# Kernel optimization log

Measured on AMD Instinct MI355X. Metric: run time of the kernel, lower is better.

Reference implementation:

```python
import jax, jax.numpy as jnp
import numpy as np

BATCH, SEQ = 2, 2048
HID = 2048          # hidden_size
INTER = 4096        # intermediate_size
STATE = 16          # ssm_state_size
RANK = 128          # time_step_rank
K = 4               # conv_kernel


def setup_inputs() -> dict:
    key = jax.random.key(0)
    ks = jax.random.split(key, 8)
    s = 0.02
    return {
        "hidden_states": jax.random.normal(ks[0], (BATCH, SEQ, HID), jnp.float32),
        "in_proj_w": jax.random.normal(ks[1], (2 * INTER, HID), jnp.float32) * s,
        "conv_w": jax.random.normal(ks[2], (INTER, 1, K), jnp.float32) * s,   # depthwise (O, I/g=1, K)
        "conv_b": jnp.zeros((INTER,), jnp.float32),
        "x_proj_w": jax.random.normal(ks[3], (RANK + 2 * STATE, INTER), jnp.float32) * s,
        "dt_proj_w": jax.random.normal(ks[4], (INTER, RANK), jnp.float32) * s,
        "dt_proj_b": jax.random.normal(ks[5], (INTER,), jnp.float32) * s,
        "A_log": jnp.log(jnp.broadcast_to(jnp.arange(1, STATE + 1, dtype=jnp.float32), (INTER, STATE))),
        "D": jnp.ones((INTER,), jnp.float32),
        "out_proj_w": jax.random.normal(ks[6], (HID, INTER), jnp.float32) * s,
    }


def reference(hidden_states, in_proj_w, conv_w, conv_b, x_proj_w,
              dt_proj_w, dt_proj_b, A_log, D, out_proj_w):
    B, L, _ = hidden_states.shape
    # in_proj -> (B, L, 2*INTER), split into u (SSM input) and gate
    proj = jnp.einsum('blh,ph->blp', hidden_states, in_proj_w)
    u, gate = jnp.split(proj, 2, axis=-1)                       # (B, L, INTER) each
    # depthwise causal conv1d on channel-major layout (B, INTER, L)
    uc = jnp.swapaxes(u, 1, 2)
    conv = jax.lax.conv_general_dilated(
        uc, conv_w, window_strides=(1,), padding=[(K - 1, 0)],
        dimension_numbers=('NCH', 'OIH', 'NCH'), feature_group_count=INTER)
    u = jax.nn.silu(conv + conv_b[None, :, None])               # (B, INTER, L)
    # x_proj: dt-rank + B + C, computed in fp32 like the original
    ssm_p = jnp.einsum('bdl,pd->blp', u, x_proj_w).astype(jnp.float32)
    dt_r, Bm, Cm = jnp.split(ssm_p, [RANK, RANK + STATE], axis=-1)  # (B,L,RANK),(B,L,N),(B,L,N)
    dt = jax.nn.softplus(jnp.einsum('blr,dr->bld', dt_r, dt_proj_w) + dt_proj_b)  # (B, L, INTER)
    A = -jnp.exp(A_log)                                         # (INTER, STATE)

    def step(state, xs):
        dt_t, B_t, C_t, u_t = xs                                # (B,D),(B,N),(B,N),(B,D)
        dA = jnp.exp(dt_t[:, :, None] * A[None])                # (B, D, N)
        state = dA * state + (dt_t * u_t)[:, :, None] * B_t[:, None, :]
        y = jnp.einsum('bdn,bn->bd', state, C_t)
        return state, y

    xs = (jnp.swapaxes(dt, 0, 1),        # (L, B, D)
          jnp.swapaxes(Bm, 0, 1),        # (L, B, N)
          jnp.swapaxes(Cm, 0, 1),        # (L, B, N)
          jnp.moveaxis(u, 2, 0))         # (L, B, D)
    init = jnp.zeros((B, INTER, STATE), jnp.float32)
    _, ys = jax.lax.scan(step, init, xs)                        # (L, B, D)

    y = jnp.moveaxis(ys, 0, 1) + jnp.swapaxes(u, 1, 2) * D[None, None, :]  # skip connection
    y = y * jax.nn.silu(gate)
    return jnp.einsum('bld,hd->blh', y, out_proj_w)             # (B, L, HID)
```

## Files before the change

### kernel.cpp

```cpp
#include <hip/hip_runtime.h>

typedef unsigned int u32;
typedef unsigned short u16;
typedef float f32x4 __attribute__((ext_vector_type(4)));
typedef float f32x16 __attribute__((ext_vector_type(16)));
typedef u16 us4 __attribute__((ext_vector_type(4)));
typedef u16 us8 __attribute__((ext_vector_type(8)));
typedef __bf16 bf16x8 __attribute__((ext_vector_type(8)));

__device__ __forceinline__ u16 f2bf(float f) {
  u32 u = __builtin_bit_cast(u32, f);
  u += 0x7fffu + ((u >> 16) & 1u);
  return (u16)(u >> 16);
}
__device__ __forceinline__ float bf2f(u16 h) {
  u32 u = ((u32)h) << 16;
  return __builtin_bit_cast(float, u);
}
__device__ __forceinline__ void async16(const void* g, void* l) {
  __builtin_amdgcn_global_load_lds((const __attribute__((address_space(1))) void*)g,
                                   (__attribute__((address_space(3))) void*)l, 16, 0, 0);
}

#define STG(GP, LP, OFF, KOFF)                              \
  {                                                         \
    async16((GP) + (KOFF), (LP) + (OFF));                   \
    async16((GP) + 128L * K + (KOFF), (LP) + (OFF) + 4096); \
  }

#define PHASE(SET, KS, MH, STAGE_STMT, TAIL_STMT)                               \
  {                                                                             \
    const u16* Ap_ = As + (SET) * 16384 + (KS) * 8192;                          \
    const u16* Bp_ = Bs + (SET) * 16384 + (KS) * 8192;                          \
    us8 af0 = *(const us8*)(Ap_ + ra[(MH) * 4 + 0]);                            \
    us8 af1 = *(const us8*)(Ap_ + ra[(MH) * 4 + 1]);                            \
    us8 af2 = *(const us8*)(Ap_ + ra[(MH) * 4 + 2]);                            \
    us8 af3 = *(const us8*)(Ap_ + ra[(MH) * 4 + 3]);                            \
    if ((MH) == 0) {                                                            \
      _Pragma("unroll") for (int nf = 0; nf < 4; ++nf)                          \
          bfr[nf] = *(const us8*)(Bp_ + rb[nf]);                                \
    }                                                                           \
    STAGE_STMT;                                                                 \
    __builtin_amdgcn_s_barrier();                                               \
    asm volatile("s_waitcnt lgkmcnt(0)" ::: "memory");                          \
    __builtin_amdgcn_sched_barrier(0);                                          \
    __builtin_amdgcn_s_setprio(1);                                              \
    _Pragma("unroll") for (int nf = 0; nf < 4; ++nf) {                          \
      acc[(MH) * 4 + 0][nf] = __builtin_amdgcn_mfma_f32_16x16x32_bf16(          \
          __builtin_bit_cast(bf16x8, af0), __builtin_bit_cast(bf16x8, bfr[nf]), \
          acc[(MH) * 4 + 0][nf], 0, 0, 0);                                      \
      acc[(MH) * 4 + 1][nf] = __builtin_amdgcn_mfma_f32_16x16x32_bf16(          \
          __builtin_bit_cast(bf16x8, af1), __builtin_bit_cast(bf16x8, bfr[nf]), \
          acc[(MH) * 4 + 1][nf], 0, 0, 0);                                      \
      acc[(MH) * 4 + 2][nf] = __builtin_amdgcn_mfma_f32_16x16x32_bf16(          \
          __builtin_bit_cast(bf16x8, af2), __builtin_bit_cast(bf16x8, bfr[nf]), \
          acc[(MH) * 4 + 2][nf], 0, 0, 0);                                      \
      acc[(MH) * 4 + 3][nf] = __builtin_amdgcn_mfma_f32_16x16x32_bf16(          \
          __builtin_bit_cast(bf16x8, af3), __builtin_bit_cast(bf16x8, bfr[nf]), \
          acc[(MH) * 4 + 3][nf], 0, 0, 0);                                      \
    }                                                                           \
    __builtin_amdgcn_s_setprio(0);                                              \
    TAIL_STMT;                                                                  \
    __builtin_amdgcn_s_barrier();                                               \
  }

__global__ __launch_bounds__(512, 2) void gemm256(const u16* __restrict__ A,
                                                  const u16* __restrict__ B,
                                                  u16* __restrict__ U,
                                                  u16* __restrict__ G, int K) {
  __shared__ __align__(16) u16 As[32768];
  __shared__ __align__(16) u16 Bs[32768];
  const int tid = threadIdx.x;
  const int lane = tid & 63;
  const int wave = tid >> 6;
  const int wm = wave >> 2;
  const int wn = wave & 3;
  const int l15 = lane & 15;
  const int kc2 = lane >> 4;
  const int pc2s = kc2 ^ ((l15 >> 1) & 3);

  const int nbx = (int)gridDim.x;
  const int d = (int)blockIdx.y * nbx + (int)blockIdx.x;
  const int cpn = nbx >> 3;
  const int xcd = d & 7;
  const int s = d >> 3;
  const long colBase = (long)(xcd * cpn + (s % cpn)) << 8;
  const long rowBase = (long)(s / cpn) << 8;

  const int c0 = ((tid & 3) ^ ((tid >> 3) & 3)) << 3;
  const u16* Ag = A + (rowBase + (tid >> 2)) * (long)K + c0;
  const u16* Bg = B + (colBase + (tid >> 2)) * (long)K + c0;
  u16* Alds = As + tid * 8;
  u16* Blds = Bs + tid * 8;

  int ra[8], rb[4];
#pragma unroll
  for (int mf = 0; mf < 8; ++mf)
    ra[mf] = (wm * 128 + mf * 16 + l15) * 32 + pc2s * 8;
#pragma unroll
  for (int nf = 0; nf < 4; ++nf)
    rb[nf] = (wn * 64 + nf * 16 + l15) * 32 + pc2s * 8;

  f32x4 acc[8][4] = {};
  us8 bfr[4];

  STG(Ag, Alds, 0, 0);
  STG(Bg, Blds, 0, 0);
  STG(Ag, Alds, 8192, 32);
  STG(Bg, Blds, 8192, 32);
  STG(Ag, Alds, 16384, 64);
  STG(Bg, Blds, 16384, 64);
  asm volatile("s_waitcnt vmcnt(4)" ::: "memory");
  __builtin_amdgcn_s_barrier();

  const int nIter = K >> 7;
  for (int t = 0; t < nIter; ++t) {
    const int k1 = (2 * t + 1) * 64;
    const int k2 = (2 * t + 2) * 64;
    const int k3 = (2 * t + 3) * 64;
    const bool full = (t < nIter - 1);
    PHASE(0, 0, 0, { STG(Ag, Alds, 24576, k1 + 32); }, {});
    PHASE(0, 0, 1, { STG(Bg, Blds, 24576, k1 + 32); },
          { asm volatile("s_waitcnt vmcnt(8)" ::: "memory"); });
    PHASE(0, 1, 0, { if (full) STG(Ag, Alds, 0, k2); }, {});
    PHASE(0, 1, 1, { if (full) STG(Bg, Blds, 0, k2); },
          {
            if (full) asm volatile("s_waitcnt vmcnt(8)" ::: "memory");
            else asm volatile("s_waitcnt vmcnt(4)" ::: "memory");
          });
    PHASE(1, 0, 0, { if (full) STG(Ag, Alds, 8192, k2 + 32); }, {});
    PHASE(1, 0, 1, { if (full) STG(Bg, Blds, 8192, k2 + 32); },
          {
            if (full) asm volatile("s_waitcnt vmcnt(8)" ::: "memory");
            else asm volatile("s_waitcnt vmcnt(0)" ::: "memory");
          });
    PHASE(1, 1, 0, { if (full) STG(Ag, Alds, 16384, k3); }, {});
    PHASE(1, 1, 1, { if (full) STG(Bg, Blds, 16384, k3); },
          { if (full) asm volatile("s_waitcnt vmcnt(8)" ::: "memory"); });
  }

  const int gate = (colBase >= 4096);
  u16* Out = gate ? G : U;
  const long cb = gate ? (colBase - 4096) : colBase;
#pragma unroll
  for (int mf = 0; mf < 8; ++mf) {
    long row0 = rowBase + wm * 128 + mf * 16 + (lane >> 4) * 4;
#pragma unroll
    for (int nf = 0; nf < 4; ++nf) {
      long col = cb + wn * 64 + nf * 16 + l15;
#pragma unroll
      for (int r = 0; r < 4; ++r) {
        float v = acc[mf][nf][r];
        if (gate) v = v / (1.f + __expf(-v));
        Out[(row0 + r) * 4096 + col] = f2bf(v);
      }
    }
  }
}

template <int ACT, bool SPLITK = false>
__global__ __launch_bounds__(256) void gemm_bt(const u16* __restrict__ A,
                                               const u16* __restrict__ B,
                                               void* __restrict__ Cv,
                                               const float* __restrict__ bias,
                                               int K, int ldc) {
  __shared__ __align__(16) u16 As[128 * 64];
  __shared__ __align__(16) u16 Bs[128 * 64];
  const int tid = threadIdx.x;
  const int lane = tid & 63;
  const int wave = tid >> 6;
  const int ln = lane & 31;
  const int hw = lane >> 5;
  const int wm = (wave >> 1) << 6;
  const int wn = (wave & 1) << 6;
  const long rowBase = (long)blockIdx.y << 7;
  const long colBase = (long)blockIdx.x << 7;

  int kStart = 0, kEnd = K;
  if constexpr (SPLITK) {
    int kn = K / gridDim.z;
    kStart = blockIdx.z * kn;
    kEnd = kStart + kn;
  }

  const int rr = tid >> 3;
  const int qg = (tid & 7) ^ (rr & 7);
  const u16* Ag = A + (rowBase + rr) * (long)K + qg * 8;
  const u16* Bg = B + (colBase + rr) * (long)K + qg * 8;
  u16* Al = As + tid * 8;
  u16* Bl = Bs + tid * 8;

  f32x16 acc[2][2] = {};
  const int l7 = ln & 7;

  for (int k0 = kStart; k0 < kEnd; k0 += 64) {
#pragma unroll
    for (int c = 0; c < 4; ++c) {
      async16(Ag + 32L * c * K + k0, Al + 2048 * c);
      async16(Bg + 32L * c * K + k0, Bl + 2048 * c);
    }
    __syncthreads();
#pragma unroll
    for (int s = 0; s < 4; ++s) {
      const int xa = ((s * 2 + hw) ^ l7) * 8;
      us8 af[2], bfr[2];
#pragma unroll
      for (int i = 0; i < 2; ++i)
        af[i] = *(const us8*)(As + (wm + i * 32 + ln) * 64 + xa);
#pragma unroll
      for (int i = 0; i < 2; ++i)
        bfr[i] = *(const us8*)(Bs + (wn + i * 32 + ln) * 64 + xa);
#pragma unroll
      for (int i = 0; i < 2; ++i)
#pragma unroll
        for (int j = 0; j < 2; ++j)
          acc[i][j] = __builtin_amdgcn_mfma_f32_32x32x16_bf16(
              __builtin_bit_cast(bf16x8, af[i]), __builtin_bit_cast(bf16x8, bfr[j]),
              acc[i][j], 0, 0, 0);
    }
    __syncthreads();
  }

  float* Cf = (float*)Cv;
  if constexpr (SPLITK)
    Cf += (size_t)blockIdx.z * ((size_t)gridDim.y * 128 * ldc);

#pragma unroll
  for (int i = 0; i < 2; ++i)
#pragma unroll
    for (int j = 0; j < 2; ++j)
#pragma unroll
      for (int r = 0; r < 16; ++r) {
        long row = rowBase + wm + i * 32 + (r & 3) + 8 * (r >> 2) + 4 * hw;
        long col = colBase + wn + j * 32 + ln;
        float v = acc[i][j][r];
        if constexpr (ACT == 0) {
          Cf[row * ldc + col] = v;
        } else if constexpr (ACT == 3) {
          v += bias[col];
          float sp = (v > 20.f) ? v : log1pf(__expf(v));
          Cf[row * ldc + col] = sp;
        } else if constexpr (ACT == 4) {
          v += bias[col];
          float sp = (v > 20.f) ? v : log1pf(__expf(v));
          ((u16*)Cv)[row * ldc + col] = f2bf(sp);
        }
      }
}

__device__ __forceinline__ void cvt4(const float* __restrict__ in,
                                     u16* __restrict__ out, int i) {
  f32x4 v = ((const f32x4*)in)[i];
  us4 o;
  o[0] = f2bf(v[0]); o[1] = f2bf(v[1]); o[2] = f2bf(v[2]); o[3] = f2bf(v[3]);
  ((us4*)out)[i] = o;
}
__global__ __launch_bounds__(256) void cvt_all(
    const float* __restrict__ hs, const float* __restrict__ wIn,
    const float* __restrict__ wOut, const float* __restrict__ wDt,
    const float* __restrict__ wX, u16* __restrict__ Xb, u16* __restrict__ Winb,
    u16* __restrict__ Wob, u16* __restrict__ Wdtb, u16* __restrict__ Wxb) {
  int i = blockIdx.x * 256 + threadIdx.x;
  if (i < 2097152) { cvt4(hs, Xb, i); return; }
  i -= 2097152;
  if (i < 4194304) { cvt4(wIn, Winb, i); return; }
  i -= 4194304;
  if (i < 2097152) { cvt4(wOut, Wob, i); return; }
  i -= 2097152;
  if (i < 131072) { cvt4(wDt, Wdtb, i); return; }
  i -= 131072;
  if (i >= 262144) return;
  int row = (i << 2) >> 12;
  us4 o;
  if (row < 160) {
    f32x4 v = ((const f32x4*)wX)[i];
    o[0] = f2bf(v[0]); o[1] = f2bf(v[1]); o[2] = f2bf(v[2]); o[3] = f2bf(v[3]);
  } else {
    o[0] = 0; o[1] = 0; o[2] = 0; o[3] = 0;
  }
  ((us4*)Wxb)[i] = o;
}

__global__ __launch_bounds__(256) void xp_reduce(const float* __restrict__ part,
                                                 float* __restrict__ smp,
                                                 u16* __restrict__ dtrb) {
  int i = blockIdx.x * 256 + threadIdx.x;
  const f32x4* p = (const f32x4*)part;
  f32x4 v = p[i];
  v += p[i + 262144];
  v += p[i + 524288];
  v += p[i + 786432];
  ((f32x4*)smp)[i] = v;
  int e = i << 2;
  int c = e & 255;
  if (c < 128) {
    int t = e >> 8;
    us4 o;
    o[0] = f2bf(v[0]); o[1] = f2bf(v[1]); o[2] = f2bf(v[2]); o[3] = f2bf(v[3]);
    *(us4*)(dtrb + t * 128 + c) = o;
  }
}

__global__ __launch_bounds__(256) void conv_silu(const u16* __restrict__ U,
                                                 const float* __restrict__ cw,
                                                 const float* __restrict__ cb,
                                                 u16* __restrict__ out) {
  int i = blockIdx.x * 256 + threadIdx.x;
  int t = i >> 10;
  int d4 = (i & 1023) << 2;
  int l = t & 2047;
  float w[4][4];
#pragma unroll
  for (int j = 0; j < 4; ++j) {
    f32x4 wv = *(const f32x4*)(cw + (d4 + j) * 4);
    w[j][0] = wv[0]; w[j][1] = wv[1]; w[j][2] = wv[2]; w[j][3] = wv[3];
  }
  float r[4] = {cb[d4], cb[d4 + 1], cb[d4 + 2], cb[d4 + 3]};
#pragma unroll
  for (int k = 0; k < 4; ++k) {
    int ll = l - 3 + k;
    if (ll >= 0) {
      us4 xv = *(const us4*)(U + (size_t)(t - 3 + k) * 4096 + d4);
      r[0] += w[0][k] * bf2f(xv[0]);
      r[1] += w[1][k] * bf2f(xv[1]);
      r[2] += w[2][k] * bf2f(xv[2]);
      r[3] += w[3][k] * bf2f(xv[3]);
    }
  }
  us4 o;
#pragma unroll
  for (int j = 0; j < 4; ++j) {
    float v = r[j];
    float s = v / (1.f + __expf(-v));
    o[j] = f2bf(s);
  }
  *(us4*)(out + (size_t)t * 4096 + d4) = o;
}

__global__ __launch_bounds__(256) void scan_part(
    const u16* __restrict__ dt, const u16* __restrict__ ub,
    const float* __restrict__ ssmp, const float* __restrict__ Alog,
    float* __restrict__ Sout, float* __restrict__ dtsumo) {
  const int tid = threadIdx.x;
  const int chunk = blockIdx.x, dgrp = blockIdx.y, b = blockIdx.z;
  const int d = (dgrp << 8) + tid;
  float A[16];
#pragma unroll
  for (int q = 0; q < 4; ++q) {
    f32x4 v = *(const f32x4*)(Alog + d * 16 + q * 4);
    A[q * 4 + 0] = -__expf(v[0]);
    A[q * 4 + 1] = -__expf(v[1]);
    A[q * 4 + 2] = -__expf(v[2]);
    A[q * 4 + 3] = -__expf(v[3]);
  }
  bool fastl = true;
#pragma unroll
  for (int n = 1; n < 16; ++n)
    fastl = fastl && (fabsf(A[n] - (n + 1) * A[0]) <= 1e-4f * (float)(n + 1));
  const bool fast = (__ballot(fastl) == ~0ull);

  const int base = b * 2048 + chunk * 64;
  const u16* dtp = dt + (size_t)base * 4096 + d;
  const u16* up = ub + (size_t)base * 4096 + d;
  const float* Bp = ssmp + (size_t)base * 256 + 128;

  float s[16] = {};
  float dtsum = 0.f;
  float cdt[8], cu[8], ndt[8] = {}, nu[8] = {};
#pragma unroll
  for (int j = 0; j < 8; ++j) {
    cdt[j] = bf2f(dtp[j * 4096]);
    cu[j] = bf2f(up[j * 4096]);
  }
  for (int l0 = 0; l0 < 64; l0 += 8) {
    if (l0 + 8 < 64) {
      int o = (l0 + 8) * 4096;
#pragma unroll
      for (int j = 0; j < 8; ++j) {
        ndt[j] = bf2f(dtp[o + j * 4096]);
        nu[j] = bf2f(up[o + j * 4096]);
      }
    }
    if (fast) {
#pragma unroll
      for (int j = 0; j < 8; ++j) {
        float e1 = __expf(cdt[j] * A[0]);
        float x = cdt[j] * cu[j];
        const float* Bl = Bp + (l0 + j) * 256;
        f32x4 B0 = *(const f32x4*)(Bl);
        f32x4 B1 = *(const f32x4*)(Bl + 4);
        f32x4 B2 = *(const f32x4*)(Bl + 8);
        f32x4 B3 = *(const f32x4*)(Bl + 12);
        float p = 1.f;
#pragma unroll
        for (int n = 0; n < 16; ++n) {
          p *= e1;
          float Bn = (n < 4) ? B0[n & 3] : (n < 8) ? B1[n & 3] : (n < 12) ? B2[n & 3] : B3[n & 3];
          s[n] = fmaf(p, s[n], x * Bn);
        }
        dtsum += cdt[j];
      }
    } else {
#pragma unroll
      for (int j = 0; j < 8; ++j) {
        float x = cdt[j] * cu[j];
        const float* Bl = Bp + (l0 + j) * 256;
        f32x4 B0 = *(const f32x4*)(Bl);
        f32x4 B1 = *(const f32x4*)(Bl + 4);
        f32x4 B2 = *(const f32x4*)(Bl + 8);
        f32x4 B3 = *(const f32x4*)(Bl + 12);
#pragma unroll
        for (int n = 0; n < 16; ++n) {
          float e = __expf(cdt[j] * A[n]);
          float Bn = (n < 4) ? B0[n & 3] : (n < 8) ? B1[n & 3] : (n < 12) ? B2[n & 3] : B3[n & 3];
          s[n] = fmaf(e, s[n], x * Bn);
        }
        dtsum += cdt[j];
      }
    }
#pragma unroll
    for (int j = 0; j < 8; ++j) { cdt[j] = ndt[j]; cu[j] = nu[j]; }
  }
  size_t o = ((size_t)(b * 32 + chunk) * 16) * 4096 + d;
#pragma unroll
  for (int n = 0; n < 16; ++n) Sout[o + (size_t)n * 4096] = s[n];
  dtsumo[(size_t)(b * 32 + chunk) * 4096 + d] = dtsum;
}

__global__ __launch_bounds__(256) void scan_fold(
    const float* __restrict__ Sin, const float* __restrict__ dtsum,
    const float* __restrict__ Alog, float* __restrict__ Sinit) {
  const int tid = threadIdx.x;
  const int n = blockIdx.x, dgrp = blockIdx.y, b = blockIdx.z;
  const int d = (dgrp << 8) + tid;
  const float A = -__expf(Alog[d * 16 + n]);
  float run = 0.f;
  for (int c = 0; c < 32; ++c) {
    size_t o = ((size_t)(b * 32 + c) * 16 + n) * 4096 + d;
    Sinit[o] = run;
    float P = __expf(dtsum[(size_t)(b * 32 + c) * 4096 + d] * A);
    run = fmaf(P, run, Sin[o]);
  }
}

__global__ __launch_bounds__(256) void scan_y(
    const u16* __restrict__ dt, const u16* __restrict__ ub,
    const float* __restrict__ ssmp, const u16* __restrict__ gs,
    const float* __restrict__ Alog, const float* __restrict__ Dv,
    const float* __restrict__ Sinit, u16* __restrict__ yb) {
  const int tid = threadIdx.x;
  const int chunk = blockIdx.x, dgrp = blockIdx.y, b = blockIdx.z;
  const int d = (dgrp << 8) + tid;
  float A[16];
#pragma unroll
  for (int q = 0; q < 4; ++q) {
    f32x4 v = *(const f32x4*)(Alog + d * 16 + q * 4);
    A[q * 4 + 0] = -__expf(v[0]);
    A[q * 4 + 1] = -__expf(v[1]);
    A[q * 4 + 2] = -__expf(v[2]);
    A[q * 4 + 3] = -__expf(v[3]);
  }
  bool fastl = true;
#pragma unroll
  for (int n = 1; n < 16; ++n)
    fastl = fastl && (fabsf(A[n] - (n + 1) * A[0]) <= 1e-4f * (float)(n + 1));
  const bool fast = (__ballot(fastl) == ~0ull);
  const float Dd = Dv[d];

  const int base = b * 2048 + chunk * 64;
  const u16* dtp = dt + (size_t)base * 4096 + d;
  const u16* up = ub + (size_t)base * 4096 + d;
  const u16* gp = gs + (size_t)base * 4096 + d;
  const float* Bp = ssmp + (size_t)base * 256 + 128;
  u16* yo = yb + (size_t)base * 4096 + d;

  float s[16];
  {
    size_t o = ((size_t)(b * 32 + chunk) * 16) * 4096 + d;
#pragma unroll
    for (int n = 0; n < 16; ++n) s[n] = Sinit[o + (size_t)n * 4096];
  }

  float cdt[8], cu[8], cg[8], ndt[8] = {}, nu[8] = {}, ng[8] = {};
#pragma unroll
  for (int j = 0; j < 8; ++j) {
    cdt[j] = bf2f(dtp[j * 4096]);
    cu[j] = bf2f(up[j * 4096]);
    cg[j] = bf2f(gp[j * 4096]);
  }
  for (int l0 = 0; l0 < 64; l0 += 8) {
    if (l0 + 8 < 64) {
      int o = (l0 + 8) * 4096;
#pragma unroll
      for (int j = 0; j < 8; ++j) {
        ndt[j] = bf2f(dtp[o + j * 4096]);
        nu[j] = bf2f(up[o + j * 4096]);
        ng[j] = bf2f(gp[o + j * 4096]);
      }
    }
    if (fast) {
#pragma unroll
      for (int j = 0; j < 8; ++j) {
        float e1 = __expf(cdt[j] * A[0]);
        float x = cdt[j] * cu[j];
        const float* Bl = Bp + (l0 + j) * 256;
        f32x4 B0 = *(const f32x4*)(Bl);
        f32x4 B1 = *(const f32x4*)(Bl + 4);
        f32x4 B2 = *(const f32x4*)(Bl + 8);
        f32x4 B3 = *(const f32x4*)(Bl + 12);
        f32x4 C0 = *(const f32x4*)(Bl + 16);
        f32x4 C1 = *(const f32x4*)(Bl + 20);
        f32x4 C2 = *(const f32x4*)(Bl + 24);
        f32x4 C3 = *(const f32x4*)(Bl + 28);
        float p = 1.f;
        float y0 = 0.f, y1 = 0.f, y2 = 0.f, y3 = 0.f;
#pragma unroll
        for (int n = 0; n < 16; ++n) {
          p *= e1;
          float Bn = (n < 4) ? B0[n & 3] : (n < 8) ? B1[n & 3] : (n < 12) ? B2[n & 3] : B3[n & 3];
          float Cn = (n < 4) ? C0[n & 3] : (n < 8) ? C1[n & 3] : (n < 12) ? C2[n & 3] : C3[n & 3];
          s[n] = fmaf(p, s[n], x * Bn);
          if (n < 4) y0 = fmaf(s[n], Cn, y0);
          else if (n < 8) y1 = fmaf(s[n], Cn, y1);
          else if (n < 12) y2 = fmaf(s[n], Cn, y2);
          else y3 = fmaf(s[n], Cn, y3);
        }
        float y = (y0 + y1) + (y2 + y3);
        yo[(l0 + j) * 4096] = f2bf((y + cu[j] * Dd) * cg[j]);
      }
    } else {
#pragma unroll
      for (int j = 0; j < 8; ++j) {
        float x = cdt[j] * cu[j];
        const float* Bl = Bp + (l0 + j) * 256;
        f32x4 B0 = *(const f32x4*)(Bl);
        f32x4 B1 = *(const f32x4*)(Bl + 4);
        f32x4 B2 = *(const f32x4*)(Bl + 8);
        f32x4 B3 = *(const f32x4*)(Bl + 12);
        f32x4 C0 = *(const f32x4*)(Bl + 16);
        f32x4 C1 = *(const f32x4*)(Bl + 20);
        f32x4 C2 = *(const f32x4*)(Bl + 24);
        f32x4 C3 = *(const f32x4*)(Bl + 28);
        float y0 = 0.f, y1 = 0.f, y2 = 0.f, y3 = 0.f;
#pragma unroll
        for (int n = 0; n < 16; ++n) {
          float e = __expf(cdt[j] * A[n]);
          float Bn = (n < 4) ? B0[n & 3] : (n < 8) ? B1[n & 3] : (n < 12) ? B2[n & 3] : B3[n & 3];
          float Cn = (n < 4) ? C0[n & 3] : (n < 8) ? C1[n & 3] : (n < 12) ? C2[n & 3] : C3[n & 3];
          s[n] = fmaf(e, s[n], x * Bn);
          if (n < 4) y0 = fmaf(s[n], Cn, y0);
          else if (n < 8) y1 = fmaf(s[n], Cn, y1);
          else if (n < 12) y2 = fmaf(s[n], Cn, y2);
          else y3 = fmaf(s[n], Cn, y3);
        }
        float y = (y0 + y1) + (y2 + y3);
        yo[(l0 + j) * 4096] = f2bf((y + cu[j] * Dd) * cg[j]);
      }
    }
#pragma unroll
    for (int j = 0; j < 8; ++j) { cdt[j] = ndt[j]; cu[j] = nu[j]; cg[j] = ng[j]; }
  }
}

extern "C" void kernel_launch(void* const* d_in, const int* in_sizes, int n_in,
                              void* d_out, int out_size, void* d_ws,
                              size_t ws_size, hipStream_t stream) {
  (void)in_sizes; (void)n_in; (void)out_size; (void)ws_size;
  const float* hs = (const float*)d_in[0];
  const float* wIn = (const float*)d_in[1];
  const float* cw = (const float*)d_in[2];
  const float* cb = (const float*)d_in[3];
  const float* wX = (const float*)d_in[4];
  const float* wDt = (const float*)d_in[5];
  const float* bDt = (const float*)d_in[6];
  const float* Alog = (const float*)d_in[7];
  const float* Dv = (const float*)d_in[8];
  const float* wOut = (const float*)d_in[9];

  const size_t MB = 1ull << 20;
  char* w = (char*)d_ws;
  u16* Xb = (u16*)(w + 0 * MB);
  u16* Winb = (u16*)(w + 16 * MB);
  u16* Pu = (u16*)(w + 48 * MB);
  u16* Dtb = (u16*)(w + 0 * MB);
  u16* Yb = (u16*)(w + 64 * MB);
  u16* Ub = (u16*)(w + 96 * MB);
  u16* Wxb = (u16*)(w + 128 * MB);
  float* Smp = (float*)(w + 130 * MB);
  u16* Dtrb = (u16*)(w + 134 * MB);
  u16* Wdtb = (u16*)(w + 135 * MB);
  u16* Wob = (u16*)(w + 136 * MB);
  float* Schk = (float*)(w + 152 * MB);
  float* Xpart = (float*)(w + 152 * MB);
  float* Sinit = (float*)(w + 168 * MB);
  float* Dtsum = (float*)(w + 184 * MB);
  u16* Pg = (u16*)d_out;

  cvt_all<<<34304, 256, 0, stream>>>(hs, wIn, wOut, wDt, wX, Xb, Winb, Wob, Wdtb, Wxb);
  gemm256<<<dim3(32, 16), 512, 0, stream>>>(Xb, Winb, Pu, Pg, 2048);
  conv_silu<<<16384, 256, 0, stream>>>(Pu, cw, cb, Ub);
  gemm_bt<0, true><<<dim3(2, 32, 4), 256, 0, stream>>>(Ub, Wxb, Xpart, nullptr, 4096, 256);
  xp_reduce<<<1024, 256, 0, stream>>>(Xpart, Smp, Dtrb);
  gemm_bt<4><<<dim3(32, 32), 256, 0, stream>>>(Dtrb, Wdtb, Dtb, bDt, 128, 4096);
  scan_part<<<dim3(32, 16, 2), 256, 0, stream>>>(Dtb, Ub, Smp, Alog, Schk, Dtsum);
  scan_fold<<<dim3(16, 16, 2), 256, 0, stream>>>(Schk, Dtsum, Alog, Sinit);
  scan_y<<<dim3(32, 16, 2), 256, 0, stream>>>(Dtb, Ub, Smp, Pg, Alog, Dv, Sinit, Yb);
  gemm_bt<0><<<dim3(16, 32), 256, 0, stream>>>(Yb, Wob, (float*)d_out, nullptr, 4096, 2048);
}
```

Baseline: 621.6 us.

## Double-buffer LDS fragment reads to prefetch next phase during MFMA

Restructures the in_proj GEMM main loop so that each phase issues LDS reads for the next phase's A/B fragments into double-buffered registers before running MFMAs on the current ones. This drops the per-phase barrier plus lgkmcnt(0) wait that came before the compute, so LDS latency can overlap with matrix math. The vmcnt thresholds are retuned to match the new ordering. The cost is more VGPRs for the fragment buffers, and if the wait counts are wrong the loop could race.

```diff
diff --git a/kernel.cpp b/kernel.cpp
--- a/kernel.cpp
+++ b/kernel.cpp
@@ -28,39 +28,42 @@
     async16((GP) + 128L * K + (KOFF), (LP) + (OFF) + 4096); \
   }
 
-#define PHASE(SET, KS, MH, STAGE_STMT, TAIL_STMT)                               \
+#define PHASE(MH, CA, CB, NSET, NKS, NMH, NA, NB, ISSB, STAGE_STMT, VMW_STMT)   \
   {                                                                             \
-    const u16* Ap_ = As + (SET) * 16384 + (KS) * 8192;                          \
-    const u16* Bp_ = Bs + (SET) * 16384 + (KS) * 8192;                          \
-    us8 af0 = *(const us8*)(Ap_ + ra[(MH) * 4 + 0]);                            \
-    us8 af1 = *(const us8*)(Ap_ + ra[(MH) * 4 + 1]);                            \
-    us8 af2 = *(const us8*)(Ap_ + ra[(MH) * 4 + 2]);                            \
-    us8 af3 = *(const us8*)(Ap_ + ra[(MH) * 4 + 3]);                            \
-    if ((MH) == 0) {                                                            \
-      _Pragma("unroll") for (int nf = 0; nf < 4; ++nf)                          \
-          bfr[nf] = *(const us8*)(Bp_ + rb[nf]);                                \
+    STAGE_STMT;                                                                 \
+    VMW_STMT;                                                                   \
+    const u16* Anp_ = As + (NSET) * 16384 + (NKS) * 8192;                       \
+    afb[NA][0] = *(const us8*)(Anp_ + ra[(NMH) * 4 + 0]);                       \
+    afb[NA][1] = *(const us8*)(Anp_ + ra[(NMH) * 4 + 1]);                       \
+    afb[NA][2] = *(const us8*)(Anp_ + ra[(NMH) * 4 + 2]);                       \
+    afb[NA][3] = *(const us8*)(Anp_ + ra[(NMH) * 4 + 3]);                       \
+    if (ISSB) {                                                                 \
+      const u16* Bnp_ = Bs + (NSET) * 16384 + (NKS) * 8192;                     \
+      bfb[NB][0] = *(const us8*)(Bnp_ + rb[0]);                                 \
+      bfb[NB][1] = *(const us8*)(Bnp_ + rb[1]);                                 \
+      bfb[NB][2] = *(const us8*)(Bnp_ + rb[2]);                                 \
+      bfb[NB][3] = *(const us8*)(Bnp_ + rb[3]);                                 \
     }                                                                           \
-    STAGE_STMT;                                                                 \
-    __builtin_amdgcn_s_barrier();                                               \
-    asm volatile("s_waitcnt lgkmcnt(0)" ::: "memory");                          \
-    __builtin_amdgcn_sched_barrier(0);                                          \
     __builtin_amdgcn_s_setprio(1);                                              \
     _Pragma("unroll") for (int nf = 0; nf < 4; ++nf) {                          \
       acc[(MH) * 4 + 0][nf] = __builtin_amdgcn_mfma_f32_16x16x32_bf16(          \
-          __builtin_bit_cast(bf16x8, af0), __builtin_bit_cast(bf16x8, bfr[nf]), \
-          acc[(MH) * 4 + 0][nf], 0, 0, 0);                                      \
+          __builtin_bit_cast(bf16x8, afb[CA][0]),                               \
+          __builtin_bit_cast(bf16x8, bfb[CB][nf]), acc[(MH) * 4 + 0][nf], 0, 0, \
+          0);                                                                   \
       acc[(MH) * 4 + 1][nf] = __builtin_amdgcn_mfma_f32_16x16x32_bf16(          \
-          __builtin_bit_cast(bf16x8, af1), __builtin_bit_cast(bf16x8, bfr[nf]), \
-          acc[(MH) * 4 + 1][nf], 0, 0, 0);                                      \
+          __builtin_bit_cast(bf16x8, afb[CA][1]),                               \
+          __builtin_bit_cast(bf16x8, bfb[CB][nf]), acc[(MH) * 4 + 1][nf], 0, 0, \
+          0);                                                                   \
       acc[(MH) * 4 + 2][nf] = __builtin_amdgcn_mfma_f32_16x16x32_bf16(          \
-          __builtin_bit_cast(bf16x8, af2), __builtin_bit_cast(bf16x8, bfr[nf]), \
-          acc[(MH) * 4 + 2][nf], 0, 0, 0);                                      \
+          __builtin_bit_cast(bf16x8, afb[CA][2]),                               \
+          __builtin_bit_cast(bf16x8, bfb[CB][nf]), acc[(MH) * 4 + 2][nf], 0, 0, \
+          0);                                                                   \
       acc[(MH) * 4 + 3][nf] = __builtin_amdgcn_mfma_f32_16x16x32_bf16(          \
-          __builtin_bit_cast(bf16x8, af3), __builtin_bit_cast(bf16x8, bfr[nf]), \
-          acc[(MH) * 4 + 3][nf], 0, 0, 0);                                      \
+          __builtin_bit_cast(bf16x8, afb[CA][3]),                               \
+          __builtin_bit_cast(bf16x8, bfb[CB][nf]), acc[(MH) * 4 + 3][nf], 0, 0, \
+          0);                                                                   \
     }                                                                           \
     __builtin_amdgcn_s_setprio(0);                                              \
-    TAIL_STMT;                                                                  \
     __builtin_amdgcn_s_barrier();                                               \
   }
 
@@ -102,7 +105,8 @@
     rb[nf] = (wn * 64 + nf * 16 + l15) * 32 + pc2s * 8;
 
   f32x4 acc[8][4] = {};
-  us8 bfr[4];
+  us8 afb[2][4];
+  us8 bfb[2][4];
 
   STG(Ag, Alds, 0, 0);
   STG(Bg, Blds, 0, 0);
@@ -110,8 +114,12 @@
   STG(Bg, Blds, 8192, 32);
   STG(Ag, Alds, 16384, 64);
   STG(Bg, Blds, 16384, 64);
-  asm volatile("s_waitcnt vmcnt(4)" ::: "memory");
+  asm volatile("s_waitcnt vmcnt(8)" ::: "memory");
   __builtin_amdgcn_s_barrier();
+#pragma unroll
+  for (int i = 0; i < 4; ++i) afb[0][i] = *(const us8*)(As + ra[i]);
+#pragma unroll
+  for (int nf = 0; nf < 4; ++nf) bfb[0][nf] = *(const us8*)(Bs + rb[nf]);
 
   const int nIter = K >> 7;
   for (int t = 0; t < nIter; ++t) {
@@ -119,24 +127,27 @@
     const int k2 = (2 * t + 2) * 64;
     const int k3 = (2 * t + 3) * 64;
     const bool full = (t < nIter - 1);
-    PHASE(0, 0, 0, { STG(Ag, Alds, 24576, k1 + 32); }, {});
-    PHASE(0, 0, 1, { STG(Bg, Blds, 24576, k1 + 32); },
-          { asm volatile("s_waitcnt vmcnt(8)" ::: "memory"); });
-    PHASE(0, 1, 0, { if (full) STG(Ag, Alds, 0, k2); }, {});
-    PHASE(0, 1, 1, { if (full) STG(Bg, Blds, 0, k2); },
+    PHASE(0, 0, 0, 0, 0, 1, 1, 0, 0, { STG(Ag, Alds, 24576, k1 + 32); },
+          { asm volatile("s_waitcnt vmcnt(6)" ::: "memory"); });
+    PHASE(1, 1, 0, 0, 1, 0, 0, 1, 1, { STG(Bg, Blds, 24576, k1 + 32); }, {});
+    PHASE(0, 0, 1, 0, 1, 1, 1, 0, 0, { if (full) STG(Ag, Alds, 0, k2); },
           {
-            if (full) asm volatile("s_waitcnt vmcnt(8)" ::: "memory");
+            if (full) asm volatile("s_waitcnt vmcnt(6)" ::: "memory");
             else asm volatile("s_waitcnt vmcnt(4)" ::: "memory");
           });
-    PHASE(1, 0, 0, { if (full) STG(Ag, Alds, 8192, k2 + 32); }, {});
-    PHASE(1, 0, 1, { if (full) STG(Bg, Blds, 8192, k2 + 32); },
+    PHASE(1, 1, 1, 1, 0, 0, 0, 0, 1, { if (full) STG(Bg, Blds, 0, k2); }, {});
+    PHASE(0, 0, 0, 1, 0, 1, 1, 0, 0,
+          { if (full) STG(Ag, Alds, 8192, k2 + 32); },
           {
-            if (full) asm volatile("s_waitcnt vmcnt(8)" ::: "memory");
+            if (full) asm volatile("s_waitcnt vmcnt(6)" ::: "memory");
             else asm volatile("s_waitcnt vmcnt(0)" ::: "memory");
           });
-    PHASE(1, 1, 0, { if (full) STG(Ag, Alds, 16384, k3); }, {});
-    PHASE(1, 1, 1, { if (full) STG(Bg, Blds, 16384, k3); },
-          { if (full) asm volatile("s_waitcnt vmcnt(8)" ::: "memory"); });
+    PHASE(1, 1, 0, 1, 1, 0, 0, 1, 1,
+          { if (full) STG(Bg, Blds, 8192, k2 + 32); }, {});
+    PHASE(0, 0, 1, 1, 1, 1, 1, 0, 0, { if (full) STG(Ag, Alds, 16384, k3); },
+          { if (full) asm volatile("s_waitcnt vmcnt(6)" ::: "memory"); });
+    PHASE(1, 1, 1, 0, 0, 0, 0, 0, 1, { if (full) STG(Bg, Blds, 16384, k3); },
+          {});
   }
 
   const int gate = (colBase >= 4096);
```

Result: no change. 627.2 us (+0.9%).

## Double-buffer LDS fragment reads in registers to overlap with MFMA in in_proj GEMM

Applied to the files above, without the earlier changes.

The main loop of the in_proj GEMM changes from eight half-phases, each with its own barrier and full lgkmcnt wait, to four phases. Each phase issues reads of the next k-slice's A/B fragments into a second register buffer while MFMAs run on the current buffer. The goal is to hide LDS read latency behind MFMA work and to halve the number of barriers per iteration. The cost is more live registers (24 us8 fragments instead of 8), which may press against the 2-blocks-per-CU launch bound. It also relies on the compiler's implicit waits being placed correctly now that the explicit lgkmcnt waits are gone.

```diff
diff --git a/kernel.cpp b/kernel.cpp
--- a/kernel.cpp
+++ b/kernel.cpp
@@ -28,40 +28,27 @@
     async16((GP) + 128L * K + (KOFF), (LP) + (OFF) + 4096); \
   }
 
-#define PHASE(SET, KS, MH, STAGE_STMT, TAIL_STMT)                               \
-  {                                                                             \
-    const u16* Ap_ = As + (SET) * 16384 + (KS) * 8192;                          \
-    const u16* Bp_ = Bs + (SET) * 16384 + (KS) * 8192;                          \
-    us8 af0 = *(const us8*)(Ap_ + ra[(MH) * 4 + 0]);                            \
-    us8 af1 = *(const us8*)(Ap_ + ra[(MH) * 4 + 1]);                            \
-    us8 af2 = *(const us8*)(Ap_ + ra[(MH) * 4 + 2]);                            \
-    us8 af3 = *(const us8*)(Ap_ + ra[(MH) * 4 + 3]);                            \
-    if ((MH) == 0) {                                                            \
-      _Pragma("unroll") for (int nf = 0; nf < 4; ++nf)                          \
-          bfr[nf] = *(const us8*)(Bp_ + rb[nf]);                                \
-    }                                                                           \
-    STAGE_STMT;                                                                 \
-    __builtin_amdgcn_s_barrier();                                               \
-    asm volatile("s_waitcnt lgkmcnt(0)" ::: "memory");                          \
-    __builtin_amdgcn_sched_barrier(0);                                          \
-    __builtin_amdgcn_s_setprio(1);                                              \
-    _Pragma("unroll") for (int nf = 0; nf < 4; ++nf) {                          \
-      acc[(MH) * 4 + 0][nf] = __builtin_amdgcn_mfma_f32_16x16x32_bf16(          \
-          __builtin_bit_cast(bf16x8, af0), __builtin_bit_cast(bf16x8, bfr[nf]), \
-          acc[(MH) * 4 + 0][nf], 0, 0, 0);                                      \
-      acc[(MH) * 4 + 1][nf] = __builtin_amdgcn_mfma_f32_16x16x32_bf16(          \
-          __builtin_bit_cast(bf16x8, af1), __builtin_bit_cast(bf16x8, bfr[nf]), \
-          acc[(MH) * 4 + 1][nf], 0, 0, 0);                                      \
-      acc[(MH) * 4 + 2][nf] = __builtin_amdgcn_mfma_f32_16x16x32_bf16(          \
-          __builtin_bit_cast(bf16x8, af2), __builtin_bit_cast(bf16x8, bfr[nf]), \
-          acc[(MH) * 4 + 2][nf], 0, 0, 0);                                      \
-      acc[(MH) * 4 + 3][nf] = __builtin_amdgcn_mfma_f32_16x16x32_bf16(          \
-          __builtin_bit_cast(bf16x8, af3), __builtin_bit_cast(bf16x8, bfr[nf]), \
-          acc[(MH) * 4 + 3][nf], 0, 0, 0);                                      \
-    }                                                                           \
-    __builtin_amdgcn_s_setprio(0);                                              \
-    TAIL_STMT;                                                                  \
-    __builtin_amdgcn_s_barrier();                                               \
+#define PHASE4(CB, NB, NSET, NKS, DOREADS, STAGE_STMT, VMW_STMT)        \
+  {                                                                     \
+    STAGE_STMT;                                                         \
+    if (DOREADS) {                                                      \
+      const u16* Anp_ = As + (NSET) * 16384 + (NKS) * 8192;             \
+      const u16* Bnp_ = Bs + (NSET) * 16384 + (NKS) * 8192;             \
+      _Pragma("unroll") for (int i = 0; i < 8; ++i)                     \
+          afb[NB][i] = *(const us8*)(Anp_ + ra[i]);                     \
+      _Pragma("unroll") for (int i = 0; i < 4; ++i)                     \
+          bfb[NB][i] = *(const us8*)(Bnp_ + rb[i]);                     \
+    }                                                                   \
+    __builtin_amdgcn_s_setprio(1);                                      \
+    _Pragma("unroll") for (int nf = 0; nf < 4; ++nf)                    \
+        _Pragma("unroll") for (int mf = 0; mf < 8; ++mf)                \
+            acc[mf][nf] = __builtin_amdgcn_mfma_f32_16x16x32_bf16(      \
+                __builtin_bit_cast(bf16x8, afb[CB][mf]),                \
+                __builtin_bit_cast(bf16x8, bfb[CB][nf]), acc[mf][nf],   \
+                0, 0, 0);                                               \
+    __builtin_amdgcn_s_setprio(0);                                      \
+    VMW_STMT;                                                           \
+    __builtin_amdgcn_s_barrier();                                       \
   }
 
 __global__ __launch_bounds__(512, 2) void gemm256(const u16* __restrict__ A,
@@ -102,7 +89,8 @@
     rb[nf] = (wn * 64 + nf * 16 + l15) * 32 + pc2s * 8;
 
   f32x4 acc[8][4] = {};
-  us8 bfr[4];
+  us8 afb[2][8];
+  us8 bfb[2][4];
 
   STG(Ag, Alds, 0, 0);
   STG(Bg, Blds, 0, 0);
@@ -112,6 +100,10 @@
   STG(Bg, Blds, 16384, 64);
   asm volatile("s_waitcnt vmcnt(4)" ::: "memory");
   __builtin_amdgcn_s_barrier();
+#pragma unroll
+  for (int i = 0; i < 8; ++i) afb[0][i] = *(const us8*)(As + ra[i]);
+#pragma unroll
+  for (int i = 0; i < 4; ++i) bfb[0][i] = *(const us8*)(Bs + rb[i]);
 
   const int nIter = K >> 7;
   for (int t = 0; t < nIter; ++t) {
@@ -119,24 +111,39 @@
     const int k2 = (2 * t + 2) * 64;
     const int k3 = (2 * t + 3) * 64;
     const bool full = (t < nIter - 1);
-    PHASE(0, 0, 0, { STG(Ag, Alds, 24576, k1 + 32); }, {});
-    PHASE(0, 0, 1, { STG(Bg, Blds, 24576, k1 + 32); },
-          { asm volatile("s_waitcnt vmcnt(8)" ::: "memory"); });
-    PHASE(0, 1, 0, { if (full) STG(Ag, Alds, 0, k2); }, {});
-    PHASE(0, 1, 1, { if (full) STG(Bg, Blds, 0, k2); },
-          {
-            if (full) asm volatile("s_waitcnt vmcnt(8)" ::: "memory");
-            else asm volatile("s_waitcnt vmcnt(4)" ::: "memory");
-          });
-    PHASE(1, 0, 0, { if (full) STG(Ag, Alds, 8192, k2 + 32); }, {});
-    PHASE(1, 0, 1, { if (full) STG(Bg, Blds, 8192, k2 + 32); },
-          {
-            if (full) asm volatile("s_waitcnt vmcnt(8)" ::: "memory");
-            else asm volatile("s_waitcnt vmcnt(0)" ::: "memory");
-          });
-    PHASE(1, 1, 0, { if (full) STG(Ag, Alds, 16384, k3); }, {});
-    PHASE(1, 1, 1, { if (full) STG(Bg, Blds, 16384, k3); },
-          { if (full) asm volatile("s_waitcnt vmcnt(8)" ::: "memory"); });
+    PHASE4(0, 1, 0, 1, true,
+           {
+             STG(Ag, Alds, 24576, k1 + 32);
+             STG(Bg, Blds, 24576, k1 + 32);
+           },
+           { asm volatile("s_waitcnt vmcnt(4)" ::: "memory"); });
+    PHASE4(1, 0, 1, 0, true,
+           {
+             if (full) {
+               STG(Ag, Alds, 0, k2);
+               STG(Bg, Blds, 0, k2);
+             }
+           },
+           {
+             if (full) asm volatile("s_waitcnt vmcnt(4)" ::: "memory");
+             else asm volatile("s_waitcnt vmcnt(0)" ::: "memory");
+           });
+    PHASE4(0, 1, 1, 1, true,
+           {
+             if (full) {
+               STG(Ag, Alds, 8192, k2 + 32);
+               STG(Bg, Blds, 8192, k2 + 32);
+             }
+           },
+           { if (full) asm volatile("s_waitcnt vmcnt(4)" ::: "memory"); });
+    PHASE4(1, 0, 0, 0, full,
+           {
+             if (full) {
+               STG(Ag, Alds, 16384, k3);
+               STG(Bg, Blds, 16384, k3);
+             }
+           },
+           { if (full) asm volatile("s_waitcnt vmcnt(4)" ::: "memory"); });
   }
 
   const int gate = (colBase >= 4096);
```

Result: slower. 925.1 us (+48.8%).
